# Kernel tuning notes

Measured on AMD Instinct MI355X. Metric: run time of the kernel, lower is better.

## Reference

```python
import jax, jax.numpy as jnp
import numpy as np

OUTCOMES = [8, 8, 8, 8, 8, 8]           # concept outcome counts (concepts_order)
N_TOTAL = int(np.prod(OUTCOMES))        # 262144 joint states
N_VALID = 8192                          # admissible states
B, D = 4096, 1024


def setup_inputs() -> dict:
    key = jax.random.key(0)
    k1, k2 = jax.random.split(key)
    embeddings = jax.random.normal(k1, (B, D), dtype=jnp.float32)
    W = jax.random.normal(k2, (N_VALID, D), dtype=jnp.float32) * 0.02
    b = jnp.zeros((N_VALID,), dtype=jnp.float32)
    # unique sorted admissible-state indices, like torch.argwhere(mask)
    rng = np.random.default_rng(0)
    valid_states = jnp.asarray(
        np.sort(rng.choice(N_TOTAL, size=N_VALID, replace=False)).astype(np.int32))
    return {"embeddings": embeddings, "W": W, "b": b, "valid_states": valid_states}


def reference(embeddings, W, b, valid_states):
    # softmax over valid states: [B, N_VALID]
    probs = jax.nn.softmax(embeddings @ W.T + b, axis=1)
    probs_t = probs.T  # [N_VALID, B] for leading-axis segment reduction
    marginals = []
    stride = N_TOTAL
    for n_i in OUTCOMES:
        stride //= n_i
        # digit of each valid joint-state index along this concept's axis
        digit = (valid_states // stride) % n_i  # [N_VALID]
        # equivalent to scattering probs into the full joint tensor and
        # summing over all other concept axes, without materializing it
        m = jax.ops.segment_sum(probs_t, digit, num_segments=n_i).T  # [B, n_i]
        marginals.append(m)
    return jnp.stack(marginals)  # [n_concepts, B, 8]
```

## Files before the change

kernel.cpp:

```cpp
#include <hip/hip_runtime.h>
#include <hip/hip_bf16.h>
#include <cstdint>
#include <cstddef>

typedef __bf16 bf16_t;
typedef bf16_t bf16x8 __attribute__((ext_vector_type(8)));
typedef bf16_t bf16x4 __attribute__((ext_vector_type(4)));
typedef float  f32x4  __attribute__((ext_vector_type(4)));
typedef unsigned int u32;

#define BROWS 4096
#define NV    8192
#define KD    1024
#define NT    16
#define ST    48
#define LOG2E 1.44269504088896340736f

#define GLL(gsrc, ldst) \
  __builtin_amdgcn_global_load_lds((const __attribute__((address_space(1))) u32*)(gsrc), \
                                   (__attribute__((address_space(3))) u32*)(ldst), 16, 0, 0)
#define FENCE asm volatile("" ::: "memory")

__global__ void prep_kernel(const float* __restrict__ E, const float* __restrict__ W,
                            const int* __restrict__ vs,
                            bf16_t* __restrict__ Eb, bf16_t* __restrict__ Wb,
                            bf16_t* __restrict__ s2t) {
  const int nE = BROWS * KD / 4;
  const int nW = NV * KD / 4;
  const int nS = ST * NV / 8;
  const int nT = nE + nW + nS;
  int idx = blockIdx.x * blockDim.x + threadIdx.x;
  int stride = gridDim.x * blockDim.x;
  for (int i = idx; i < nT; i += stride) {
    if (i < nE + nW) {
      const float4* s; bf16x4* d; int j;
      if (i < nE) { s = (const float4*)E; d = (bf16x4*)Eb; j = i; }
      else        { s = (const float4*)W; d = (bf16x4*)Wb; j = i - nE; }
      float4 v = s[j];
      bf16x4 o;
      o[0] = (bf16_t)v.x; o[1] = (bf16_t)v.y; o[2] = (bf16_t)v.z; o[3] = (bf16_t)v.w;
      d[j] = o;
    } else {
      int u  = i - nE - nW;
      int b  = u >> 10;
      int i0 = (u & 1023) * 8;
      int base = i0 ^ ((b & 7) << 3);
      int c = b >> 3, d = b & 7, sh = 15 - 3 * c;
      bf16x8 o;
#pragma unroll
      for (int e = 0; e < 8; ++e)
        o[e] = (bf16_t)((((vs[base + e] >> sh) & 7) == d) ? 1.0f : 0.0f);
      *(bf16x8*)(s2t + (size_t)b * NV + i0) = o;
    }
  }
}

__global__ __launch_bounds__(512, 2)
void gemm_fused_kernel(const bf16_t* __restrict__ W, const bf16_t* __restrict__ E,
                       const float* __restrict__ bias, const bf16_t* __restrict__ s2t,
                       float* __restrict__ part) {
  __shared__ __align__(16) char lds[2][65536];
  #define AKH0 0
  #define AKH1 16384
  #define BKH0 32768
  #define BKH1 49152

  const int t    = threadIdx.x;
  const int lane = t & 63;
  const int wv   = t >> 6;
  const int wm   = wv >> 2;
  const int wn   = wv & 3;
  const int fr   = lane & 15;
  const int fq   = lane >> 4;

  int bid = blockIdx.x;
  int wg  = (bid & 7) * 64 + (bid >> 3);
  const int stile = wg >> 4;
  const int btile = wg & 15;
  const int st0 = stile * 256;
  const int bt0 = btile * 256;

  const int srow = lane >> 2;
  const int skel = ((lane & 3) ^ ((lane >> 3) & 3)) * 8;
  const bf16_t* aptr = W + (size_t)(st0 + wv * 32 + srow) * KD + skel;
  const bf16_t* bptr = E + (size_t)(bt0 + wv * 32 + srow) * KD + skel;
  const int dchunk = (wv * 2) * 1024;

  const int xsw    = (fr & 6) << 3;
  const int a_base = wm * 8192 + ((fr * 64 + fq * 16) ^ xsw);
  const int b_base = wn * 4096 + ((fr * 64 + fq * 16) ^ xsw);

  f32x4 acc[8][4] = {};

  GLL(aptr,                &lds[0][AKH0 + dchunk]);
  GLL(aptr + 16 * KD,      &lds[0][AKH0 + dchunk + 1024]);
  GLL(bptr,                &lds[0][BKH0 + dchunk]);
  GLL(bptr + 16 * KD,      &lds[0][BKH0 + dchunk + 1024]);
  GLL(aptr + 32,           &lds[0][AKH1 + dchunk]);
  GLL(aptr + 32 + 16 * KD, &lds[0][AKH1 + dchunk + 1024]);
  GLL(bptr + 32,           &lds[0][BKH1 + dchunk]);
  GLL(bptr + 32 + 16 * KD, &lds[0][BKH1 + dchunk + 1024]);
  asm volatile("s_waitcnt vmcnt(0)" ::: "memory");
  __builtin_amdgcn_s_barrier();
  FENCE;

  int cur = 0;
  for (int kt = 0; kt < NT; ++kt) {
    const char* bufp = lds[cur];
    char* nbuf = lds[cur ^ 1];
    const bool pf = (kt + 1 < NT);

    bf16x8 a0[8], b0[4], a1[8], b1[4];

#pragma unroll
    for (int n = 0; n < 4; ++n)
      b0[n] = *(const bf16x8*)(bufp + b_base + BKH0 + n * 1024);
#pragma unroll
    for (int m = 0; m < 8; ++m)
      a0[m] = *(const bf16x8*)(bufp + a_base + AKH0 + m * 1024);

    if (pf) {
      const bf16_t* an = aptr + (kt + 1) * 64;
      const bf16_t* bn = bptr + (kt + 1) * 64;
      GLL(an,                &nbuf[AKH0 + dchunk]);
      GLL(an + 16 * KD,      &nbuf[AKH0 + dchunk + 1024]);
      GLL(bn,                &nbuf[BKH0 + dchunk]);
      GLL(bn + 16 * KD,      &nbuf[BKH0 + dchunk + 1024]);
      GLL(an + 32,           &nbuf[AKH1 + dchunk]);
      GLL(an + 32 + 16 * KD, &nbuf[AKH1 + dchunk + 1024]);
      GLL(bn + 32,           &nbuf[BKH1 + dchunk]);
      GLL(bn + 32 + 16 * KD, &nbuf[BKH1 + dchunk + 1024]);
    }

#pragma unroll
    for (int n = 0; n < 4; ++n)
      b1[n] = *(const bf16x8*)(bufp + b_base + BKH1 + n * 1024);
#pragma unroll
    for (int m = 0; m < 8; ++m)
      a1[m] = *(const bf16x8*)(bufp + a_base + AKH1 + m * 1024);

    __builtin_amdgcn_s_setprio(1);
#pragma unroll
    for (int m = 0; m < 8; ++m)
#pragma unroll
      for (int n = 0; n < 4; ++n)
        acc[m][n] = __builtin_amdgcn_mfma_f32_16x16x32_bf16(a0[m], b0[n], acc[m][n], 0, 0, 0);
#pragma unroll
    for (int m = 0; m < 8; ++m)
#pragma unroll
      for (int n = 0; n < 4; ++n)
        acc[m][n] = __builtin_amdgcn_mfma_f32_16x16x32_bf16(a1[m], b1[n], acc[m][n], 0, 0, 0);
    __builtin_amdgcn_s_setprio(0);

    asm volatile("s_waitcnt vmcnt(0)" ::: "memory");
    __builtin_amdgcn_sched_barrier(0);
    __builtin_amdgcn_s_barrier();
    FENCE;
    cur ^= 1;
  }

  char* const ldsf = &lds[0][0];
  {
#pragma unroll
    for (int q = 0; q < 3; ++q) {
      const bf16_t* src = s2t + (size_t)(wv * 6 + q * 2 + (lane >> 5)) * NV
                          + st0 + (lane & 31) * 8;
      GLL(src, ldsf + 65536 + wv * 3072 + q * 1024);
    }
  }

  float* const ppart = part + (size_t)bt0 * (32 * ST) + (size_t)stile * ST;

#pragma unroll
  for (int pass = 0; pass < 2; ++pass) {
    if ((wn >> 1) == pass) {
#pragma unroll
      for (int m = 0; m < 8; ++m) {
        const float4 bb = *(const float4*)&bias[st0 + wm * 128 + m * 16 + fq * 4];
#pragma unroll
        for (int n = 0; n < 4; ++n) {
          bf16x4 ev;
          ev[0] = (bf16_t)exp2f((acc[m][n][0] + bb.x) * LOG2E);
          ev[1] = (bf16_t)exp2f((acc[m][n][1] + bb.y) * LOG2E);
          ev[2] = (bf16_t)exp2f((acc[m][n][2] + bb.z) * LOG2E);
          ev[3] = (bf16_t)exp2f((acc[m][n][3] + bb.w) * LOG2E);
          const int jh = (wn & 1) * 64 + n * 16 + fr;
          const int ib = (wm * 128 + m * 16 + fq * 4) * 2;
          *(bf16x4*)(ldsf + jh * 512 + (ib ^ ((fr & 7) << 4))) = ev;
        }
      }
    }
    if (pass == 0) asm volatile("s_waitcnt vmcnt(0)" ::: "memory");
    __syncthreads();

    f32x4 acc2[3] = {{0.f,0.f,0.f,0.f},{0.f,0.f,0.f,0.f},{0.f,0.f,0.f,0.f}};
#pragma unroll
    for (int k2 = 0; k2 < 8; ++k2) {
      const int ko2 = (k2 * 64 + fq * 16) ^ ((fr & 7) << 4);
      const bf16x8 ea = *(const bf16x8*)(ldsf + (wv * 16 + fr) * 512 + ko2);
#pragma unroll
      for (int n2 = 0; n2 < 3; ++n2) {
        const bf16x8 sb = *(const bf16x8*)(ldsf + 65536 + (n2 * 16 + fr) * 512 + ko2);
        acc2[n2] = __builtin_amdgcn_mfma_f32_16x16x32_bf16(ea, sb, acc2[n2], 0, 0, 0);
      }
    }
    const int jg = pass * 128 + wv * 16 + fq * 4;
#pragma unroll
    for (int n2 = 0; n2 < 3; ++n2)
#pragma unroll
      for (int r = 0; r < 4; ++r)
        ppart[(size_t)(jg + r) * (32 * ST) + n2 * 16 + fr] = acc2[n2][r];
    __syncthreads();
  }
}

__global__ __launch_bounds__(256)
void reduce_kernel(const float* __restrict__ part, float* __restrict__ out) {
  const int w    = threadIdx.x >> 6;
  const int lane = threadIdx.x & 63;
  const int b    = blockIdx.x * 4 + w;

  const float* p = part + (size_t)b * (32 * ST);
  float s = 0.f;
#pragma unroll
  for (int it = 0; it < 24; ++it)
    s += p[it * 64 + lane];
  __shared__ float red[4][ST];
  if (lane < ST) red[w][lane] = 0.f;
  __syncthreads();
  if (lane < ST) {
    float acc = 0.f;
#pragma unroll
    for (int mt = 0; mt < 32; ++mt)
      acc += p[mt * ST + lane];
    red[w][lane] = acc;
  }
  __syncthreads();
  if (lane < ST) {
    const float* fin = red[w];
    float total = fin[0] + fin[1] + fin[2] + fin[3] + fin[4] + fin[5] + fin[6] + fin[7];
    out[(size_t)(lane >> 3) * BROWS * 8 + (size_t)b * 8 + (lane & 7)] = red[w][lane] / total;
  }
}

extern "C" void kernel_launch(void* const* d_in, const int* in_sizes, int n_in,
                              void* d_out, int out_size, void* d_ws, size_t ws_size,
                              hipStream_t stream) {
  const float* E    = (const float*)d_in[0];
  const float* W    = (const float*)d_in[1];
  const float* bias = (const float*)d_in[2];
  const int*   vs   = (const int*)d_in[3];
  float* out = (float*)d_out;

  char* ws = (char*)d_ws;
  size_t off = 0;
  bf16_t* Eb   = (bf16_t*)(ws + off); off += (size_t)BROWS * KD * 2;
  bf16_t* Wb   = (bf16_t*)(ws + off); off += (size_t)NV * KD * 2;
  bf16_t* s2t  = (bf16_t*)(ws + off); off += (size_t)ST * NV * 2;
  float*  part = (float*)(ws + off);  off += (size_t)BROWS * 32 * ST * 4;

  prep_kernel<<<3072, 256, 0, stream>>>(E, W, vs, Eb, Wb, s2t);
  gemm_fused_kernel<<<512, 512, 0, stream>>>(Wb, Eb, bias, s2t, part);
  reduce_kernel<<<BROWS / 4, 256, 0, stream>>>(part, out);
}
```

Measured before the change: 99.23 us.

## Load W fragments directly from global into registers, halve K-tile, shrink LDS

The GEMM main loop no longer stages the W (A) operand through LDS. Each wave now reads its A fragments straight from global memory into registers, and only the embedding (B) tile is double-buffered in LDS. The K step drops from 64 to 32, so the loop runs 32 iterations instead of 16, and the LDS footprint shrinks to 88KB. The aim is to cut LDS traffic and shared-memory size. In exchange, the four waves that share a row block now load the same W data redundantly, the direct loads are consumed in the same iteration with little latency hiding, and the number of barriers doubles. A dead partial sum and an extra barrier are also removed from the reduce kernel.

```diff
diff --git a/kernel.cpp b/kernel.cpp
--- a/kernel.cpp
+++ b/kernel.cpp
@@ -12,7 +12,7 @@
 #define BROWS 4096
 #define NV    8192
 #define KD    1024
-#define NT    16
+#define NT    32
 #define ST    48
 #define LOG2E 1.44269504088896340736f
 
@@ -59,11 +59,7 @@
 void gemm_fused_kernel(const bf16_t* __restrict__ W, const bf16_t* __restrict__ E,
                        const float* __restrict__ bias, const bf16_t* __restrict__ s2t,
                        float* __restrict__ part) {
-  __shared__ __align__(16) char lds[2][65536];
-  #define AKH0 0
-  #define AKH1 16384
-  #define BKH0 32768
-  #define BKH1 49152
+  __shared__ __align__(16) char lds[90112];
 
   const int t    = threadIdx.x;
   const int lane = t & 63;
@@ -82,74 +78,49 @@
 
   const int srow = lane >> 2;
   const int skel = ((lane & 3) ^ ((lane >> 3) & 3)) * 8;
-  const bf16_t* aptr = W + (size_t)(st0 + wv * 32 + srow) * KD + skel;
   const bf16_t* bptr = E + (size_t)(bt0 + wv * 32 + srow) * KD + skel;
-  const int dchunk = (wv * 2) * 1024;
+  const int dchunk = wv * 2048;
 
   const int xsw    = (fr & 6) << 3;
-  const int a_base = wm * 8192 + ((fr * 64 + fq * 16) ^ xsw);
   const int b_base = wn * 4096 + ((fr * 64 + fq * 16) ^ xsw);
 
+  const bf16_t* aBase = W + (size_t)(st0 + wm * 128 + fr) * KD + fq * 8;
+
   f32x4 acc[8][4] = {};
 
-  GLL(aptr,                &lds[0][AKH0 + dchunk]);
-  GLL(aptr + 16 * KD,      &lds[0][AKH0 + dchunk + 1024]);
-  GLL(bptr,                &lds[0][BKH0 + dchunk]);
-  GLL(bptr + 16 * KD,      &lds[0][BKH0 + dchunk + 1024]);
-  GLL(aptr + 32,           &lds[0][AKH1 + dchunk]);
-  GLL(aptr + 32 + 16 * KD, &lds[0][AKH1 + dchunk + 1024]);
-  GLL(bptr + 32,           &lds[0][BKH1 + dchunk]);
-  GLL(bptr + 32 + 16 * KD, &lds[0][BKH1 + dchunk + 1024]);
+  GLL(bptr,           &lds[dchunk]);
+  GLL(bptr + 16 * KD, &lds[dchunk + 1024]);
   asm volatile("s_waitcnt vmcnt(0)" ::: "memory");
   __builtin_amdgcn_s_barrier();
   FENCE;
 
   int cur = 0;
   for (int kt = 0; kt < NT; ++kt) {
-    const char* bufp = lds[cur];
-    char* nbuf = lds[cur ^ 1];
+    const char* bufp = &lds[cur * 16384];
+    char* nbuf = &lds[(cur ^ 1) * 16384];
     const bool pf = (kt + 1 < NT);
 
-    bf16x8 a0[8], b0[4], a1[8], b1[4];
+    bf16x8 a[8], b[4];
+
+#pragma unroll
+    for (int m = 0; m < 8; ++m)
+      a[m] = *(const bf16x8*)(aBase + (size_t)m * 16 * KD + kt * 32);
+
+    if (pf) {
+      GLL(bptr + (kt + 1) * 32,           &nbuf[dchunk]);
+      GLL(bptr + (kt + 1) * 32 + 16 * KD, &nbuf[dchunk + 1024]);
+    }
 
 #pragma unroll
     for (int n = 0; n < 4; ++n)
-      b0[n] = *(const bf16x8*)(bufp + b_base + BKH0 + n * 1024);
+      b[n] = *(const bf16x8*)(bufp + b_base + n * 1024);
+
+    __builtin_amdgcn_s_setprio(1);
 #pragma unroll
     for (int m = 0; m < 8; ++m)
-      a0[m] = *(const bf16x8*)(bufp + a_base + AKH0 + m * 1024);
-
-    if (pf) {
-      const bf16_t* an = aptr + (kt + 1) * 64;
-      const bf16_t* bn = bptr + (kt + 1) * 64;
-      GLL(an,                &nbuf[AKH0 + dchunk]);
-      GLL(an + 16 * KD,      &nbuf[AKH0 + dchunk + 1024]);
-      GLL(bn,                &nbuf[BKH0 + dchunk]);
-      GLL(bn + 16 * KD,      &nbuf[BKH0 + dchunk + 1024]);
-      GLL(an + 32,           &nbuf[AKH1 + dchunk]);
-      GLL(an + 32 + 16 * KD, &nbuf[AKH1 + dchunk + 1024]);
-      GLL(bn + 32,           &nbuf[BKH1 + dchunk]);
-      GLL(bn + 32 + 16 * KD, &nbuf[BKH1 + dchunk + 1024]);
-    }
-
-#pragma unroll
-    for (int n = 0; n < 4; ++n)
-      b1[n] = *(const bf16x8*)(bufp + b_base + BKH1 + n * 1024);
-#pragma unroll
-    for (int m = 0; m < 8; ++m)
-      a1[m] = *(const bf16x8*)(bufp + a_base + AKH1 + m * 1024);
-
-    __builtin_amdgcn_s_setprio(1);
-#pragma unroll
-    for (int m = 0; m < 8; ++m)
 #pragma unroll
       for (int n = 0; n < 4; ++n)
-        acc[m][n] = __builtin_amdgcn_mfma_f32_16x16x32_bf16(a0[m], b0[n], acc[m][n], 0, 0, 0);
-#pragma unroll
-    for (int m = 0; m < 8; ++m)
-#pragma unroll
-      for (int n = 0; n < 4; ++n)
-        acc[m][n] = __builtin_amdgcn_mfma_f32_16x16x32_bf16(a1[m], b1[n], acc[m][n], 0, 0, 0);
+        acc[m][n] = __builtin_amdgcn_mfma_f32_16x16x32_bf16(a[m], b[n], acc[m][n], 0, 0, 0);
     __builtin_amdgcn_s_setprio(0);
 
     asm volatile("s_waitcnt vmcnt(0)" ::: "memory");
@@ -159,7 +130,7 @@
     cur ^= 1;
   }
 
-  char* const ldsf = &lds[0][0];
+  char* const ldsf = &lds[0];
   {
 #pragma unroll
     for (int q = 0; q < 3; ++q) {
@@ -221,13 +192,7 @@
   const int b    = blockIdx.x * 4 + w;
 
   const float* p = part + (size_t)b * (32 * ST);
-  float s = 0.f;
-#pragma unroll
-  for (int it = 0; it < 24; ++it)
-    s += p[it * 64 + lane];
   __shared__ float red[4][ST];
-  if (lane < ST) red[w][lane] = 0.f;
-  __syncthreads();
   if (lane < ST) {
     float acc = 0.f;
 #pragma unroll
```

Measured after the change: 199.3 us. +100.8%, slower.
